# Kernel tuning notes

Measured on AMD Instinct MI355X. Metric: run time of the kernel, lower is better.

Reference implementation:

```python
import jax, jax.numpy as jnp
import numpy as np

B, C, H, W, L, R = 1, 32, 96, 128, 2, 3
N = 2 * R + 1
EPS = 1e-5


def conv2d(x, w, stride=1, pad=1):
    return jax.lax.conv_general_dilated(
        x, w, (stride, stride), ((pad, pad), (pad, pad)),
        dimension_numbers=('NCHW', 'OIHW', 'NCHW'))


def conv_transpose2d(x, w, stride=2, pad=1):
    # torch ConvTranspose2d semantics; w: [Cin, Cout, kH, kW]
    kh, kw = w.shape[2], w.shape[3]
    wf = jnp.flip(w, (2, 3)).transpose(1, 0, 2, 3)  # [Cout, Cin, kh, kw]
    return jax.lax.conv_general_dilated(
        x, wf, (1, 1),
        ((kh - 1 - pad, kh - 1 - pad), (kw - 1 - pad, kw - 1 - pad)),
        lhs_dilation=(stride, stride),
        dimension_numbers=('NCHW', 'OIHW', 'NCHW'))


def bnorm(x, s, b, m, v):
    # inference-mode BatchNorm2d (fixed running stats)
    inv = s * jax.lax.rsqrt(v + EPS)
    return x * inv[None, :, None, None] + (b - m * inv)[None, :, None, None]


def grid_sample(img, grid):
    # bilinear, align_corners=True, padding_mode='zeros'
    # img [B,C,H,W], grid [B,Hg,Wg,2] (x,y) in [-1,1]
    Bi, Ci, Hi, Wi = img.shape
    gx = (grid[..., 0] + 1.0) * 0.5 * (Wi - 1)
    gy = (grid[..., 1] + 1.0) * 0.5 * (Hi - 1)
    x0 = jnp.floor(gx)
    y0 = jnp.floor(gy)
    wx = (gx - x0)[:, None]  # [B,1,Hg,Wg]
    wy = (gy - y0)[:, None]

    def tap(yf, xf):
        valid = (xf >= 0) & (xf <= Wi - 1) & (yf >= 0) & (yf <= Hi - 1)
        xc = jnp.clip(xf, 0, Wi - 1).astype(jnp.int32)
        yc = jnp.clip(yf, 0, Hi - 1).astype(jnp.int32)
        v = jax.vmap(lambda im, y, x: im[:, y, x])(img, yc, xc)  # [B,C,Hg,Wg]
        return v * valid[:, None].astype(img.dtype)

    v00 = tap(y0, x0)
    v01 = tap(y0, x0 + 1)
    v10 = tap(y0 + 1, x0)
    v11 = tap(y0 + 1, x0 + 1)
    return (v00 * (1 - wx) * (1 - wy) + v01 * wx * (1 - wy)
            + v10 * (1 - wx) * wy + v11 * wx * wy)


def _forward(fmap1_0, fmap1_1, fmap2_0, fmap2_1, coords,
             cw1, cw2, cw3, cw4, ctw5, cw6, cb6,
             bn1s, bn1b, bn1m, bn1v, bn2s, bn2b, bn2m, bn2v,
             bn3s, bn3b, bn3m, bn3v, bn4s, bn4b, bn4m, bn4v,
             bn5s, bn5b, bn5m, bn5v, dap_w):
    n = N
    dx = jnp.linspace(-R, R, n)
    delta = jnp.stack(jnp.meshgrid(dx, dx, indexing='ij'), axis=-1)  # [n,n,2]
    b, _, h, w = coords.shape
    cp = coords.transpose(0, 2, 3, 1)  # [b,h,w,2] (x,y)
    bns = ((bn1s, bn1b, bn1m, bn1v), (bn2s, bn2b, bn2m, bn2v),
           (bn3s, bn3b, bn3m, bn3v), (bn4s, bn4b, bn4m, bn4v),
           (bn5s, bn5b, bn5m, bn5v))
    out = []
    for i, (f1, f2) in enumerate(((fmap1_0, fmap2_0), (fmap1_1, fmap2_1))):
        c, h2, w2 = f1.shape[1], f1.shape[2], f1.shape[3]
        # [b,n,h,n,w,2]: first n axis pairs with h, second with w (as in torch view)
        cent = cp[:, None, :, None, :, :] / (2.0 ** i) + delta[None, :, None, :, None, :]
        gx = 2.0 * cent[..., 0] / (w2 - 1) - 1.0
        gy = 2.0 * cent[..., 1] / (h2 - 1) - 1.0
        grid = jnp.stack([gx, gy], -1).reshape(b, n * h, n * w, 2)
        f2s = grid_sample(f2, grid).reshape(b, c, n, h, n, w)
        f2s = f2s.transpose(0, 2, 4, 1, 3, 5)  # [b,du,dv,c,h,w]
        f1e = jnp.broadcast_to(f1[:, None, None], (b, n, n, c, h, w))
        x = jnp.concatenate([f1e, f2s], axis=3).reshape(b * n * n, 2 * c, h, w)
        # MatchingNet (DICL): conv-bn-relu stack, stride-2 down + transposed up
        x = jax.nn.relu(bnorm(conv2d(x, cw1[i]), *(p[i] for p in bns[0])))
        x = jax.nn.relu(bnorm(conv2d(x, cw2[i], stride=2), *(p[i] for p in bns[1])))
        x = jax.nn.relu(bnorm(conv2d(x, cw3[i]), *(p[i] for p in bns[2])))
        x = jax.nn.relu(bnorm(conv2d(x, cw4[i]), *(p[i] for p in bns[3])))
        x = jax.nn.relu(bnorm(conv_transpose2d(x, ctw5[i]), *(p[i] for p in bns[4])))
        x = conv2d(x, cw6[i]) + cb6[i][None, :, None, None]  # [b*n*n,1,h,w]
        cost = x.reshape(b, n * n, h, w)
        # DisplacementAwareProjection: 1x1 conv over the 49 displacement channels
        cost = jnp.einsum('pq,bqhw->bphw', dap_w[i], cost)
        out.append(cost)
    return jnp.concatenate(out, axis=1)  # [b, L*(2r+1)^2, h, w]


def setup_inputs():
    key = jax.random.key(0)
    ks = jax.random.split(key, 40)

    def rn(k, shape, scale=1.0):
        return jax.random.normal(k, shape, jnp.float32) * scale

    inp = {}
    inp['fmap1_0'] = rn(ks[0], (B, C, H, W))
    inp['fmap2_0'] = rn(ks[1], (B, C, H, W))
    inp['fmap1_1'] = rn(ks[2], (B, C, H, W))
    inp['fmap2_1'] = rn(ks[3], (B, C, H, W))
    gy, gx = jnp.meshgrid(jnp.arange(H, dtype=jnp.float32),
                          jnp.arange(W, dtype=jnp.float32), indexing='ij')
    base = jnp.stack([gx, gy], 0)[None]  # [1,2,H,W] (x,y) pixel coords
    inp['coords'] = base + rn(ks[4], (B, 2, H, W), 2.0)

    def cw(k, co, ci, kk):
        return rn(k, (L, co, ci, kk, kk), 1.0 / np.sqrt(ci * kk * kk))

    inp['cw1'] = cw(ks[5], 96, 2 * C, 3)
    inp['cw2'] = cw(ks[6], 128, 96, 3)
    inp['cw3'] = cw(ks[7], 128, 128, 3)
    inp['cw4'] = cw(ks[8], 64, 128, 3)
    inp['ctw5'] = rn(ks[9], (L, 64, 32, 4, 4), 1.0 / np.sqrt(64 * 16))
    inp['cw6'] = cw(ks[10], 1, 32, 3)
    inp['cb6'] = rn(ks[11], (L, 1), 0.1)
    for j, ch in enumerate((96, 128, 128, 64, 32), start=1):
        k4 = jax.random.split(ks[11 + j], 4)
        inp['bn%ds' % j] = 1.0 + rn(k4[0], (L, ch), 0.1)
        inp['bn%db' % j] = rn(k4[1], (L, ch), 0.1)
        inp['bn%dm' % j] = rn(k4[2], (L, ch), 0.1)
        inp['bn%dv' % j] = 1.0 + rn(k4[3], (L, ch), 0.1) ** 2
    # DAP identity init
    inp['dap_w'] = jnp.tile(jnp.eye(N * N, dtype=jnp.float32)[None], (L, 1, 1))
    return inp


def reference(fmap1_0, fmap1_1, fmap2_0, fmap2_1, coords,
              cw1, cw2, cw3, cw4, ctw5, cw6, cb6,
              bn1s, bn1b, bn1m, bn1v, bn2s, bn2b, bn2m, bn2v,
              bn3s, bn3b, bn3m, bn3v, bn4s, bn4b, bn4m, bn4v,
              bn5s, bn5b, bn5m, bn5v, dap_w):
    return _forward(fmap1_0, fmap1_1, fmap2_0, fmap2_1, coords,
                    cw1, cw2, cw3, cw4, ctw5, cw6, cb6,
                    bn1s, bn1b, bn1m, bn1v, bn2s, bn2b, bn2m, bn2v,
                    bn3s, bn3b, bn3m, bn3v, bn4s, bn4b, bn4m, bn4v,
                    bn5s, bn5b, bn5m, bn5v, dap_w)
```

## Files before the change

kernel.cpp:

```cpp
#include <hip/hip_runtime.h>

#define EPSF 1e-5f

typedef __attribute__((ext_vector_type(8))) short short8;
typedef __attribute__((ext_vector_type(4))) float f32x4;

__device__ __forceinline__ ushort f2bf(float x) {
    union { float f; unsigned u; } c; c.f = x;
    unsigned r = c.u + 0x7FFF + ((c.u >> 16) & 1);
    return (ushort)(r >> 16);
}
__device__ __forceinline__ float bf2f(ushort b) {
    union { unsigned u; float f; } c; c.u = ((unsigned)b) << 16;
    return c.f;
}
__device__ __forceinline__ int swz(int a) {
    return a ^ (((a >> 7) & 7) << 4);
}


__global__ __launch_bounds__(256) void k_repack_conv(
    const float* __restrict__ src, ushort* __restrict__ dst, int CO, int CI)
{
    int idx = blockIdx.x * 256 + threadIdx.x;
    if (idx >= CO * CI * 9) return;
    int co = idx / (CI * 9);
    int rem = idx % (CI * 9);
    int ci = rem / 9, tap = rem % 9;
    dst[((size_t)tap * CO + co) * CI + ci] = f2bf(src[idx]);
}

__global__ __launch_bounds__(256) void k_repack_ct(
    const float* __restrict__ src, ushort* __restrict__ dst)
{
    int idx = blockIdx.x * 256 + threadIdx.x;
    if (idx >= 4 * 4 * 32 * 64) return;
    int ci = idx & 63;
    int t = idx >> 6;
    int co = t & 31; t >>= 5;
    int tap = t & 3;
    int parity = t >> 2;
    int ph = parity >> 1, pw = parity & 1;
    int a = tap >> 1, b = tap & 1;
    int kh = ((ph + 1) & 1) + 2 * a;
    int kw = ((pw + 1) & 1) + 2 * b;
    dst[idx] = f2bf(src[((ci * 32 + co) * 4 + kh) * 4 + kw]);
}

__global__ __launch_bounds__(256) void k_pack_f1(
    const float* __restrict__ f1_0, const float* __restrict__ f1_1,
    ushort* __restrict__ xf1)
{
    const int sp = blockIdx.x * 256 + threadIdx.x;
    const int l = blockIdx.z;
    const float* f1 = l ? f1_1 : f1_0;
    ushort* dst = xf1 + (size_t)l * 393216 + (size_t)sp * 32;
    #pragma unroll
    for (int g = 0; g < 4; ++g) {
        uint4 pk;
        uint* pw_ = (uint*)&pk;
        #pragma unroll
        for (int q = 0; q < 4; ++q) {
            int c = g * 8 + q * 2;
            pw_[q] = (uint)f2bf(f1[(size_t)c * 12288 + sp])
                   | ((uint)f2bf(f1[(size_t)(c + 1) * 12288 + sp]) << 16);
        }
        *(uint4*)(dst + g * 8) = pk;
    }
}

__global__ __launch_bounds__(256) void k_sample_nhwc(
    const float* __restrict__ f2_0, const float* __restrict__ f2_1,
    const float* __restrict__ coords, ushort* __restrict__ x0s, int d0)
{
    const int HW = 12288;
    const int sp = blockIdx.x * 256 + threadIdx.x;
    const int slot = blockIdx.z;
    const int p = d0 + slot;
    const int l = p / 49;
    const int d = p - l * 49;
    const int du = d / 7, dv = d % 7;
    const float inv_scale = l ? 0.5f : 1.0f;
    const float* f2 = l ? f2_1 : f2_0;

    float cx = coords[sp] * inv_scale + (float)(du - 3);
    float cy = coords[HW + sp] * inv_scale + (float)(dv - 3);
    float xf = floorf(cx), yf = floorf(cy);
    float wx = cx - xf, wy = cy - yf;
    int xi = (int)xf, yi = (int)yf;
    float vx0 = (xf >= 0.f && xf <= 127.f) ? 1.f : 0.f;
    float vx1 = (xf + 1.f >= 0.f && xf + 1.f <= 127.f) ? 1.f : 0.f;
    float vy0 = (yf >= 0.f && yf <= 95.f) ? 1.f : 0.f;
    float vy1 = (yf + 1.f >= 0.f && yf + 1.f <= 95.f) ? 1.f : 0.f;
    int x0i = min(max(xi, 0), 127), x1i = min(max(xi + 1, 0), 127);
    int y0i = min(max(yi, 0), 95),  y1i = min(max(yi + 1, 0), 95);
    float w00 = (1.f - wx) * (1.f - wy) * vx0 * vy0;
    float w01 = wx * (1.f - wy) * vx1 * vy0;
    float w10 = (1.f - wx) * wy * vx0 * vy1;
    float w11 = wx * wy * vx1 * vy1;
    int o00 = y0i * 128 + x0i, o01 = y0i * 128 + x1i;
    int o10 = y1i * 128 + x0i, o11 = y1i * 128 + x1i;

    ushort* dst = x0s + ((size_t)slot * HW + sp) * 32;
    #pragma unroll
    for (int g = 0; g < 4; ++g) {
        uint4 pk;
        uint* pw_ = (uint*)&pk;
        #pragma unroll
        for (int q = 0; q < 4; ++q) {
            uint wv = 0;
            #pragma unroll
            for (int h = 0; h < 2; ++h) {
                int c = g * 8 + q * 2 + h;
                const float* fc = f2 + (size_t)c * HW;
                float s = w00 * fc[o00] + w01 * fc[o01] + w10 * fc[o10] + w11 * fc[o11];
                wv |= ((uint)f2bf(s)) << (16 * h);
            }
            pw_[q] = wv;
        }
        *(uint4*)(dst + g * 8) = pk;
    }
}

template <int EPI>
__global__ __launch_bounds__(512, 2) void k_conv1(
    const ushort* __restrict__ in,
    ushort* __restrict__ out,
    const ushort* __restrict__ wbase,
    const float* __restrict__ p1,
    const float* __restrict__ bs0, const float* __restrict__ bb0,
    const float* __restrict__ bm0, const float* __restrict__ bv0,
    int d0, int koff)
{
    constexpr int AB = 10 * 66 * 64;
    constexpr int PB = 3 * 48 * 64;
    constexpr int SA = 6;
    __shared__ __align__(16) char smem[AB + 2 * PB];
    char* As = smem;

    const int tid = threadIdx.x;
    const int lane = tid & 63, wid = tid >> 6;
    const int lr = lane & 15, kg = lane >> 4;
    const int bx = blockIdx.x;
    const int rt = bx >> 1, ct = bx & 1;
    const int r0 = rt * 8, c0 = ct * 64;
    const int y = blockIdx.y;
    const int co0 = y * 48;
    const int slot = blockIdx.z;
    const int l = EPI ? slot : (d0 + slot) / 49;

    const ushort* ib = in + (size_t)slot * 12288 * 32;
    const ushort* wl = wbase + (size_t)l * (9 * 96 * 64);
    const short8 z8 = {0, 0, 0, 0, 0, 0, 0, 0};

    #pragma unroll
    for (int i = 0; i < SA; ++i) {
        int lin = i * 8192 + tid * 16;
        if (lin < AB) {
            int pos = lin >> 6;
            int prow = (pos * 994) >> 16;
            int pcol = pos - prow * 66;
            int grow = r0 - 1 + prow, gcol = c0 - 1 + pcol;
            bool ok = ((unsigned)grow < 96u) && ((unsigned)gcol < 128u);
            short8 v = z8;
            if (ok) v = *(const short8*)(ib + (grow * 128 + gcol) * 32 + ((lin & 63) >> 1));
            *(short8*)(As + swz(lin)) = v;
        }
    }

    int boff[2]; unsigned bmask = 0;
    #pragma unroll
    for (int i = 0; i < 2; ++i) {
        int lin = i * 8192 + tid * 16;
        if (lin < PB) bmask |= 1u << i;
        int lc = min(lin, PB - 16);
        int rowidx = lc >> 6;
        int tpg = rowidx / 48;
        int r = rowidx - tpg * 48;
        boff[i] = (tpg * 96 + co0 + r) * 64 + koff + ((lc & 63) >> 1);
    }
    short8 stgB[2];
    auto loadB = [&](int pg) {
        const ushort* src = wl + pg * (3 * 96 * 64);
        #pragma unroll
        for (int i = 0; i < 2; ++i)
            if ((bmask >> i) & 1) stgB[i] = *(const short8*)(src + boff[i]);
    };
    auto writeB = [&](int pg) {
        char* Bs = smem + AB + (pg & 1) * PB;
        #pragma unroll
        for (int i = 0; i < 2; ++i) {
            int lin = i * 8192 + tid * 16;
            if ((bmask >> i) & 1) *(short8*)(Bs + swz(lin)) = stgB[i];
        }
    };

    f32x4 acc[4][3];
    if constexpr (EPI == 0) {
        const float* pl = p1 + (size_t)l * 1179648
                        + ((size_t)((bx * 2 + y) * 512 + tid)) * 48;
        #pragma unroll
        for (int mf = 0; mf < 4; ++mf)
            #pragma unroll
            for (int nf = 0; nf < 3; ++nf)
                acc[mf][nf] = *(const f32x4*)(pl + (mf * 3 + nf) * 4);
    } else {
        #pragma unroll
        for (int mf = 0; mf < 4; ++mf)
            #pragma unroll
            for (int nf = 0; nf < 3; ++nf)
                acc[mf][nf] = (f32x4){0.f, 0.f, 0.f, 0.f};
    }

    loadB(0);
    writeB(0);
    __syncthreads();

    #pragma unroll
    for (int ps = 0; ps < 3; ++ps) {
        if (ps < 2) loadB(ps + 1);
        const char* Bs = smem + AB + (ps & 1) * PB;
        #pragma unroll
        for (int kw = 0; kw < 3; ++kw) {
            short8 a[4];
            #pragma unroll
            for (int mf = 0; mf < 4; ++mf) {
                int sp = (wid + ps) * 66 + mf * 16 + lr + kw;
                a[mf] = *(const short8*)(As + swz(sp * 64 + kg * 16));
            }
            #pragma unroll
            for (int nf = 0; nf < 3; ++nf) {
                short8 b = *(const short8*)(Bs + swz((kw * 48 + nf * 16 + lr) * 64 + kg * 16));
                #pragma unroll
                for (int mf = 0; mf < 4; ++mf)
                    acc[mf][nf] = __builtin_amdgcn_mfma_f32_16x16x32_bf16(
                        a[mf], b, acc[mf][nf], 0, 0, 0);
            }
        }
        __syncthreads();
        if (ps < 2) { writeB(ps + 1); __syncthreads(); }
    }

    if constexpr (EPI == 1) {
        float* of = (float*)out + (size_t)l * 1179648
                  + ((size_t)((bx * 2 + y) * 512 + tid)) * 48;
        #pragma unroll
        for (int mf = 0; mf < 4; ++mf)
            #pragma unroll
            for (int nf = 0; nf < 3; ++nf)
                *(f32x4*)(of + (mf * 3 + nf) * 4) = acc[mf][nf];
    } else {
        const float* bs = bs0 + l * 96;
        const float* bb = bb0 + l * 96;
        const float* bm = bm0 + l * 96;
        const float* bv = bv0 + l * 96;
        ushort* ob = out + (size_t)slot * 12288 * 96;
        const int orow = r0 + wid;
        #pragma unroll
        for (int nf = 0; nf < 3; ++nf) {
            const int col = co0 + nf * 16 + lr;
            const float inv = bs[col] * rsqrtf(bv[col] + EPSF);
            const float beta = bb[col] - bm[col] * inv;
            #pragma unroll
            for (int mf = 0; mf < 4; ++mf) {
                #pragma unroll
                for (int j = 0; j < 4; ++j) {
                    int ocol = c0 + mf * 16 + kg * 4 + j;
                    float yv = fmaxf(fmaf(acc[mf][nf][j], inv, beta), 0.f);
                    ob[((size_t)orow * 128 + ocol) * 96 + col] = f2bf(yv);
                }
            }
        }
    }
}

template <int CIN, int COUT, int IH, int IW>
__global__ __launch_bounds__(512, 4) void k_conv_lds8s(
    const ushort* __restrict__ in, ushort* __restrict__ out,
    const ushort* __restrict__ wbase, int wlstride,
    const float* __restrict__ bs0, const float* __restrict__ bb0,
    const float* __restrict__ bm0, const float* __restrict__ bv0, int d0)
{
    constexpr int CCs = CIN / 32;
    constexpr int AB = 10 * 66 * 64;
    constexpr int PB = 3 * 64 * 64;
    constexpr int SA = 6, SB = 2;
    constexpr int NPH = 3 * CCs;
    __shared__ __align__(16) char smem[AB + 2 * PB];
    char* As = smem;

    const int tid = threadIdx.x;
    const int lane = tid & 63, wid = tid >> 6;
    const int lr = lane & 15, kg = lane >> 4;
    const int r0 = (int)blockIdx.x * 8;
    const int co0 = (int)blockIdx.y * 64;
    const int slot = blockIdx.z;
    const int l = (d0 + slot) / 49;

    int aoff[SA]; unsigned awr = 0, avalid = 0;
    #pragma unroll
    for (int i = 0; i < SA; ++i) {
        int lin = i * 8192 + tid * 16;
        bool wr = lin < AB;
        int linc = wr ? lin : 0;
        int pos = linc >> 6;
        int prow = (pos * 994) >> 16;
        int pcol = pos - prow * 66;
        int grow = r0 - 1 + prow, gcol = pcol - 1;
        bool ok = wr && ((unsigned)grow < (unsigned)IH) && ((unsigned)gcol < (unsigned)IW);
        if (wr) awr |= 1u << i;
        if (ok) avalid |= 1u << i;
        int growc = min(max(grow, 0), IH - 1), gcolc = min(max(gcol, 0), IW - 1);
        aoff[i] = (growc * IW + gcolc) * CIN + ((linc & 63) >> 1);
    }
    int boff[SB]; unsigned bmask = 0;
    #pragma unroll
    for (int i = 0; i < SB; ++i) {
        int lin = i * 8192 + tid * 16;
        if (lin < PB) bmask |= 1u << i;
        int lc = min(lin, PB - 16);
        int rowidx = lc >> 6;
        int tpg = rowidx >> 6, r = rowidx & 63;
        boff[i] = (tpg * COUT + co0 + r) * CIN + ((lc & 63) >> 1);
    }

    const ushort* ib = in + (size_t)slot * IH * IW * CIN;
    const ushort* wl = wbase + (size_t)l * wlstride;
    const short8 z8 = {0, 0, 0, 0, 0, 0, 0, 0};

    auto stageA = [&](int cc) {
        #pragma unroll
        for (int i = 0; i < SA; ++i) {
            int lin = i * 8192 + tid * 16;
            if ((awr >> i) & 1) {
                short8 v = z8;
                if ((avalid >> i) & 1)
                    v = *(const short8*)(ib + aoff[i] + cc * 32);
                *(short8*)(As + swz(lin)) = v;
            }
        }
    };
    short8 stgB[SB];
    auto loadB = [&](int ps) {
        int pg = ps % 3, cc = ps / 3;
        const ushort* src = wl + pg * (3 * COUT * CIN) + cc * 32;
        #pragma unroll
        for (int i = 0; i < SB; ++i)
            if ((bmask >> i) & 1) stgB[i] = *(const short8*)(src + boff[i]);
    };
    auto writeB = [&](int ps) {
        char* Bs = smem + AB + (ps & 1) * PB;
        #pragma unroll
        for (int i = 0; i < SB; ++i) {
            int lin = i * 8192 + tid * 16;
            if ((bmask >> i) & 1) *(short8*)(Bs + swz(lin)) = stgB[i];
        }
    };

    f32x4 acc[4][4];
    #pragma unroll
    for (int mf = 0; mf < 4; ++mf)
        #pragma unroll
        for (int nf = 0; nf < 4; ++nf)
            acc[mf][nf] = (f32x4){0.f, 0.f, 0.f, 0.f};

    stageA(0);
    loadB(0); writeB(0);
    __syncthreads();

    #pragma unroll 1
    for (int ps = 0; ps < NPH; ++ps) {
        const int pg = ps % 3;
        const bool hasNext = (ps + 1 < NPH);
        if (hasNext) loadB(ps + 1);

        const char* Bs = smem + AB + (ps & 1) * PB;
        #pragma unroll
        for (int kw = 0; kw < 3; ++kw) {
            short8 a[4];
            #pragma unroll
            for (int mf = 0; mf < 4; ++mf) {
                int sp = (wid + pg) * 66 + mf * 16 + lr + kw;
                a[mf] = *(const short8*)(As + swz(sp * 64 + kg * 16));
            }
            #pragma unroll
            for (int nf = 0; nf < 4; ++nf) {
                short8 b = *(const short8*)(Bs + swz((kw * 64 + nf * 16 + lr) * 64 + kg * 16));
                #pragma unroll
                for (int mf = 0; mf < 4; ++mf)
                    acc[mf][nf] = __builtin_amdgcn_mfma_f32_16x16x32_bf16(
                        a[mf], b, acc[mf][nf], 0, 0, 0);
            }
        }

        __syncthreads();
        if (hasNext) {
            writeB(ps + 1);
            if (pg == 2) stageA(ps / 3 + 1);
            __syncthreads();
        }
    }

    const float* bs = bs0 + l * COUT;
    const float* bb = bb0 + l * COUT;
    const float* bm = bm0 + l * COUT;
    const float* bv = bv0 + l * COUT;
    ushort* ob = out + (size_t)slot * IH * IW * COUT;
    const int orow = r0 + wid;
    #pragma unroll
    for (int nf = 0; nf < 4; ++nf) {
        const int col = co0 + nf * 16 + lr;
        const float inv = bs[col] * rsqrtf(bv[col] + EPSF);
        const float beta = bb[col] - bm[col] * inv;
        #pragma unroll
        for (int mf = 0; mf < 4; ++mf) {
            #pragma unroll
            for (int j = 0; j < 4; ++j) {
                int ocol = mf * 16 + kg * 4 + j;
                float y = fmaxf(fmaf(acc[mf][nf][j], inv, beta), 0.f);
                ob[((size_t)orow * IW + ocol) * COUT + col] = f2bf(y);
            }
        }
    }
}

__global__ __launch_bounds__(512, 4) void k_conv_s2_8(
    const ushort* __restrict__ in, ushort* __restrict__ out,
    const ushort* __restrict__ wbase, int wlstride,
    const float* __restrict__ bs0, const float* __restrict__ bb0,
    const float* __restrict__ bm0, const float* __restrict__ bv0, int d0)
{
    constexpr int AB = 9 * 66 * 64;
    constexpr int PB = 3 * 128 * 64;
    constexpr int SA = 5;
    constexpr int SB = 3;
    constexpr int NPH = 9;
    __shared__ __align__(16) char smem[AB + PB];
    char* As = smem;

    const int tid = threadIdx.x;
    const int lane = tid & 63, wid = tid >> 6;
    const int lr = lane & 15, kg = lane >> 4;
    const int mw = wid >> 2;
    const int cw = wid & 3;
    const int bx = blockIdx.x;
    const int rt = bx >> 1, ct = bx & 1;
    const int r0 = rt * 4, oc0 = ct * 32;
    const int slot = blockIdx.z;
    const int l = (d0 + slot) / 49;

    int aoff[SA]; unsigned awr = 0, avalid = 0;
    #pragma unroll
    for (int i = 0; i < SA; ++i) {
        int lin = i * 8192 + tid * 16;
        bool wr = lin < AB;
        int linc = wr ? lin : 0;
        int pos = linc >> 6;
        int prow = (pos * 994) >> 16;
        int pcol = pos - prow * 66;
        int grow = 2 * r0 - 1 + prow, gcol = 2 * oc0 - 1 + pcol;
        bool ok = wr && ((unsigned)grow < 96u) && ((unsigned)gcol < 128u);
        if (wr) awr |= 1u << i;
        if (ok) avalid |= 1u << i;
        int growc = min(max(grow, 0), 95), gcolc = min(max(gcol, 0), 127);
        aoff[i] = (growc * 128 + gcolc) * 96 + ((linc & 63) >> 1);
    }
    int boff[SB];
    #pragma unroll
    for (int i = 0; i < SB; ++i) {
        int lin = i * 8192 + tid * 16;
        int rowidx = lin >> 6;
        int tpg = rowidx >> 7, r = rowidx & 127;
        boff[i] = (tpg * 128 + r) * 96 + ((lin & 63) >> 1);
    }

    const ushort* ib = in + (size_t)slot * 12288 * 96;
    const ushort* wl = wbase + (size_t)l * wlstride;
    const short8 z8 = {0, 0, 0, 0, 0, 0, 0, 0};

    auto stageA = [&](int cc) {
        #pragma unroll
        for (int i = 0; i < SA; ++i) {
            int lin = i * 8192 + tid * 16;
            if ((awr >> i) & 1) {
                short8 v = z8;
                if ((avalid >> i) & 1)
                    v = *(const short8*)(ib + aoff[i] + cc * 32);
                *(short8*)(As + swz(lin)) = v;
            }
        }
    };
    short8 stgB[SB];
    auto loadB = [&](int ps) {
        int pg = ps % 3, cc = ps / 3;
        const ushort* src = wl + pg * (3 * 128 * 96) + cc * 32;
        #pragma unroll
        for (int i = 0; i < SB; ++i)
            stgB[i] = *(const short8*)(src + boff[i]);
    };
    auto writeB = [&]() {
        char* Bs = smem + AB;
        #pragma unroll
        for (int i = 0; i < SB; ++i) {
            int lin = i * 8192 + tid * 16;
            *(short8*)(Bs + swz(lin)) = stgB[i];
        }
    };

    f32x4 acc[4][2];
    #pragma unroll
    for (int mf = 0; mf < 4; ++mf)
        #pragma unroll
        for (int nf = 0; nf < 2; ++nf)
            acc[mf][nf] = (f32x4){0.f, 0.f, 0.f, 0.f};

    stageA(0);
    loadB(0); writeB();
    __syncthreads();

    #pragma unroll 1
    for (int ps = 0; ps < NPH; ++ps) {
        const int pg = ps % 3;
        const bool hasNext = (ps + 1 < NPH);
        if (hasNext) loadB(ps + 1);

        const char* Bs = smem + AB;
        #pragma unroll
        for (int kw = 0; kw < 3; ++kw) {
            short8 a[4];
            #pragma unroll
            for (int mf = 0; mf < 4; ++mf) {
                int pos = (2 * (mw * 2 + (mf >> 1)) + pg) * 66
                        + 2 * ((mf & 1) * 16 + lr) + kw;
                a[mf] = *(const short8*)(As + swz(pos * 64 + kg * 16));
            }
            #pragma unroll
            for (int nf = 0; nf < 2; ++nf) {
                int rb = kw * 128 + cw * 32 + nf * 16 + lr;
                short8 b = *(const short8*)(Bs + swz(rb * 64 + kg * 16));
                #pragma unroll
                for (int mf = 0; mf < 4; ++mf)
                    acc[mf][nf] = __builtin_amdgcn_mfma_f32_16x16x32_bf16(
                        a[mf], b, acc[mf][nf], 0, 0, 0);
            }
        }

        __syncthreads();
        if (hasNext) {
            writeB();
            if (pg == 2) stageA(ps / 3 + 1);
            __syncthreads();
        }
    }

    const float* bs = bs0 + l * 128;
    const float* bb = bb0 + l * 128;
    const float* bm = bm0 + l * 128;
    const float* bv = bv0 + l * 128;
    ushort* ob = out + (size_t)slot * 3072 * 128;
    #pragma unroll
    for (int nf = 0; nf < 2; ++nf) {
        const int col = cw * 32 + nf * 16 + lr;
        const float inv = bs[col] * rsqrtf(bv[col] + EPSF);
        const float beta = bb[col] - bm[col] * inv;
        #pragma unroll
        for (int mf = 0; mf < 4; ++mf) {
            const int orow = r0 + mw * 2 + (mf >> 1);
            #pragma unroll
            for (int j = 0; j < 4; ++j) {
                int ocol = oc0 + (mf & 1) * 16 + kg * 4 + j;
                float y = fmaxf(fmaf(acc[mf][nf][j], inv, beta), 0.f);
                ob[((size_t)orow * 64 + ocol) * 128 + col] = f2bf(y);
            }
        }
    }
}

__global__ __launch_bounds__(512, 4) void k_convt_lds(
    const ushort* __restrict__ in, ushort* __restrict__ out,
    const ushort* __restrict__ wbase,
    const float* __restrict__ bs0, const float* __restrict__ bb0,
    const float* __restrict__ bm0, const float* __restrict__ bv0, int d0)
{
    constexpr int AB = 10 * 66 * 64;
    constexpr int PB = 4 * 32 * 64;
    constexpr int SA = 6;
    __shared__ __align__(16) char smem[AB + 2 * PB];
    char* As = smem;

    const int tid = threadIdx.x;
    const int lane = tid & 63, wid = tid >> 6;
    const int lr = lane & 15, kg = lane >> 4;
    const int q0 = (int)blockIdx.x * 8;
    const int parity = blockIdx.y;
    const int ph = parity >> 1, pw = parity & 1;
    const int slot = blockIdx.z;
    const int l = (d0 + slot) / 49;

    int aoff[SA]; unsigned awr = 0, avalid = 0;
    #pragma unroll
    for (int i = 0; i < SA; ++i) {
        int lin = i * 8192 + tid * 16;
        bool wr = lin < AB;
        int linc = wr ? lin : 0;
        int pos = linc >> 6;
        int prow = (pos * 994) >> 16;
        int pcol = pos - prow * 66;
        int grow = q0 - 1 + prow, gcol = pcol - 1;
        bool ok = wr && ((unsigned)grow < 48u) && ((unsigned)gcol < 64u);
        if (wr) awr |= 1u << i;
        if (ok) avalid |= 1u << i;
        int growc = min(max(grow, 0), 47), gcolc = min(max(gcol, 0), 63);
        aoff[i] = (growc * 64 + gcolc) * 64 + ((linc & 63) >> 1);
    }
    int boffB;
    {
        int lin = tid * 16;
        int rowidx = lin >> 6;
        int tap = rowidx >> 5, co = rowidx & 31;
        boffB = ((parity * 4 + tap) * 32 + co) * 64 + ((lin & 63) >> 1);
    }

    const ushort* ib = in + (size_t)slot * 3072 * 64;
    const ushort* wl = wbase + (size_t)l * (16 * 32 * 64);
    const short8 z8 = {0, 0, 0, 0, 0, 0, 0, 0};

    auto stageA = [&](int cc) {
        #pragma unroll
        for (int i = 0; i < SA; ++i) {
            int lin = i * 8192 + tid * 16;
            if ((awr >> i) & 1) {
                short8 v = z8;
                if ((avalid >> i) & 1)
                    v = *(const short8*)(ib + aoff[i] + cc * 32);
                *(short8*)(As + swz(lin)) = v;
            }
        }
    };
    short8 stgB;
    auto loadB = [&](int cc) {
        stgB = *(const short8*)(wl + boffB + cc * 32);
    };
    auto writeB = [&](int cc) {
        char* Bs = smem + AB + (cc & 1) * PB;
        *(short8*)(Bs + swz(tid * 16)) = stgB;
    };

    f32x4 acc[4][2];
    #pragma unroll
    for (int mf = 0; mf < 4; ++mf)
        #pragma unroll
        for (int nf = 0; nf < 2; ++nf)
            acc[mf][nf] = (f32x4){0.f, 0.f, 0.f, 0.f};

    stageA(0);
    loadB(0); writeB(0);
    __syncthreads();

    #pragma unroll 1
    for (int cc = 0; cc < 2; ++cc) {
        if (cc == 0) loadB(1);
        const char* Bs = smem + AB + (cc & 1) * PB;
        #pragma unroll
        for (int a = 0; a < 2; ++a) {
            #pragma unroll
            for (int b2 = 0; b2 < 2; ++b2) {
                const int tap = a * 2 + b2;
                short8 av[4];
                #pragma unroll
                for (int mf = 0; mf < 4; ++mf) {
                    int pos = (wid + 1 + ph - a) * 66 + mf * 16 + lr + pw - b2 + 1;
                    av[mf] = *(const short8*)(As + swz(pos * 64 + kg * 16));
                }
                #pragma unroll
                for (int nf = 0; nf < 2; ++nf) {
                    short8 b = *(const short8*)(Bs
                        + swz((tap * 32 + nf * 16 + lr) * 64 + kg * 16));
                    #pragma unroll
                    for (int mf = 0; mf < 4; ++mf)
                        acc[mf][nf] = __builtin_amdgcn_mfma_f32_16x16x32_bf16(
                            av[mf], b, acc[mf][nf], 0, 0, 0);
                }
            }
        }
        __syncthreads();
        if (cc == 0) {
            writeB(1);
            stageA(1);
            __syncthreads();
        }
    }

    const float* bs = bs0 + l * 32;
    const float* bb = bb0 + l * 32;
    const float* bm = bm0 + l * 32;
    const float* bv = bv0 + l * 32;
    ushort* ob = out + (size_t)slot * 12288 * 32;
    const size_t rowb = (size_t)(2 * (q0 + wid) + ph) * 128;
    #pragma unroll
    for (int nf = 0; nf < 2; ++nf) {
        const int col = nf * 16 + lr;
        const float inv = bs[col] * rsqrtf(bv[col] + EPSF);
        const float beta = bb[col] - bm[col] * inv;
        #pragma unroll
        for (int mf = 0; mf < 4; ++mf) {
            #pragma unroll
            for (int j = 0; j < 4; ++j) {
                int r = mf * 16 + kg * 4 + j;
                float y = fmaxf(fmaf(acc[mf][nf][j], inv, beta), 0.f);
                ob[(rowb + 2 * r + pw) * 32 + col] = f2bf(y);
            }
        }
    }
}

__global__ __launch_bounds__(256) void k_conv6(
    const ushort* __restrict__ x5, float* __restrict__ cost,
    const float* __restrict__ w0, const float* __restrict__ cb6, int d0)
{
    const int sp = blockIdx.x * 256 + threadIdx.x;
    const int slot = blockIdx.z;
    const int p = d0 + slot;
    const int l = p / 49;
    const float* w = w0 + l * 288;
    const int oh = sp >> 7, ow = sp & 127;
    float acc = 0.f;
    #pragma unroll
    for (int kh = 0; kh < 3; ++kh) {
        const int ih = oh - 1 + kh;
        if (ih < 0 || ih >= 96) continue;
        #pragma unroll
        for (int kw = 0; kw < 3; ++kw) {
            const int iw = ow - 1 + kw;
            if (iw < 0 || iw >= 128) continue;
            const ushort* q = x5 + ((size_t)slot * 12288 + ih * 128 + iw) * 32;
            const int tap = kh * 3 + kw;
            #pragma unroll
            for (int g = 0; g < 4; ++g) {
                uint4 v = *(const uint4*)(q + g * 8);
                const uint* vw = (const uint*)&v;
                #pragma unroll
                for (int t = 0; t < 4; ++t) {
                    int ci = g * 8 + t * 2;
                    acc = fmaf(bf2f((ushort)(vw[t] & 0xFFFF)), w[ci * 9 + tap], acc);
                    acc = fmaf(bf2f((ushort)(vw[t] >> 16)), w[(ci + 1) * 9 + tap], acc);
                }
            }
        }
    }
    cost[(size_t)p * 12288 + sp] = acc + cb6[l];
}

__global__ __launch_bounds__(256) void k_dap(
    const float* __restrict__ cost, const float* __restrict__ dw,
    float* __restrict__ out)
{
    const int sp = blockIdx.x * 256 + threadIdx.x;
    const int p = blockIdx.y;
    const float* dr = dw + p * 49;
    float acc = 0.f;
    #pragma unroll
    for (int q = 0; q < 49; ++q)
        acc = fmaf(dr[q], cost[(size_t)q * 12288 + sp], acc);
    out[(size_t)p * 12288 + sp] = acc;
}

extern "C" void kernel_launch(void* const* d_in, const int* in_sizes, int n_in,
                              void* d_out, int out_size, void* d_ws, size_t ws_size,
                              hipStream_t stream)
{
    const float* fm1_0 = (const float*)d_in[0];
    const float* fm2_0 = (const float*)d_in[1];
    const float* fm1_1 = (const float*)d_in[2];
    const float* fm2_1 = (const float*)d_in[3];
    const float* coords = (const float*)d_in[4];
    const float* cw1  = (const float*)d_in[5];
    const float* cw2  = (const float*)d_in[6];
    const float* cw3  = (const float*)d_in[7];
    const float* cw4  = (const float*)d_in[8];
    const float* ctw5 = (const float*)d_in[9];
    const float* cw6  = (const float*)d_in[10];
    const float* cb6  = (const float*)d_in[11];
    const float* bn[5][4];
    for (int j = 0; j < 5; ++j)
        for (int k = 0; k < 4; ++k)
            bn[j][k] = (const float*)d_in[12 + j * 4 + k];
    const float* dap = (const float*)d_in[32];
    float* out = (float*)d_out;

    const size_t A_US = 393216;
    const size_t B_US = 1179648;
    const size_t XF1 = 2 * 393216;
    const size_t W1 = 9 * 96 * 64, W2 = 9 * 128 * 96, W3 = 9 * 128 * 128;
    const size_t W4 = 9 * 64 * 128, W5 = 16 * 32 * 64;
    const size_t W_US = 2 * (W1 + W2 + W3 + W4 + W5);
    const size_t P1F = 2 * (size_t)24 * 2 * 512 * 48;
    const size_t COSTF = (size_t)98 * 12288;

    int DC = 1;
    for (int cand : {98, 66, 49, 42, 33, 25, 17, 13, 9, 7, 5, 3, 2, 1}) {
        size_t need = (A_US + B_US) * (size_t)cand * 2 + (XF1 + W_US) * 2
                    + (P1F + COSTF) * 4 + 4096;
        if (need <= ws_size) { DC = cand; break; }
    }

    ushort* bufA = (ushort*)d_ws;
    ushort* bufB = bufA + A_US * DC;
    ushort* xf1 = bufB + B_US * DC;
    ushort* wp = xf1 + XF1;
    ushort* wr1 = wp; wp += 2 * W1;
    ushort* wr2 = wp; wp += 2 * W2;
    ushort* wr3 = wp; wp += 2 * W3;
    ushort* wr4 = wp; wp += 2 * W4;
    ushort* wr5 = wp; wp += 2 * W5;
    float* P1 = (float*)wp;
    float* cost = P1 + P1F;

    for (int l = 0; l < 2; ++l) {
        k_repack_conv<<<dim3(216), 256, 0, stream>>>(cw1 + (size_t)l * W1, wr1 + l * W1, 96, 64);
        k_repack_conv<<<dim3(432), 256, 0, stream>>>(cw2 + (size_t)l * W2, wr2 + l * W2, 128, 96);
        k_repack_conv<<<dim3(576), 256, 0, stream>>>(cw3 + (size_t)l * W3, wr3 + l * W3, 128, 128);
        k_repack_conv<<<dim3(288), 256, 0, stream>>>(cw4 + (size_t)l * W4, wr4 + l * W4, 64, 128);
        k_repack_ct<<<dim3(128), 256, 0, stream>>>(ctw5 + (size_t)l * W5, wr5 + l * W5);
    }

    k_pack_f1<<<dim3(48, 1, 2), 256, 0, stream>>>(fm1_0, fm1_1, xf1);
    k_conv1<1><<<dim3(24, 2, 2), 512, 0, stream>>>(
        xf1, (ushort*)P1, wr1, nullptr,
        bn[0][0], bn[0][1], bn[0][2], bn[0][3], 0, 0);

    for (int d0 = 0; d0 < 98; d0 += DC) {
        const int ndd = min(DC, 98 - d0);
        k_sample_nhwc<<<dim3(48, 1, ndd), 256, 0, stream>>>(
            fm2_0, fm2_1, coords, bufA, d0);
        k_conv1<0><<<dim3(24, 2, ndd), 512, 0, stream>>>(
            bufA, bufB, wr1, P1,
            bn[0][0], bn[0][1], bn[0][2], bn[0][3], d0, 32);
        k_conv_s2_8<<<dim3(24, 1, ndd), 512, 0, stream>>>(bufB, bufA, wr2, (int)W2,
                bn[1][0], bn[1][1], bn[1][2], bn[1][3], d0);
        k_conv_lds8s<128, 128, 48, 64>
            <<<dim3(6, 2, ndd), 512, 0, stream>>>(bufA, bufB, wr3, (int)W3,
                bn[2][0], bn[2][1], bn[2][2], bn[2][3], d0);
        k_conv_lds8s<128, 64, 48, 64>
            <<<dim3(6, 1, ndd), 512, 0, stream>>>(bufB, bufA, wr4, (int)W4,
                bn[3][0], bn[3][1], bn[3][2], bn[3][3], d0);
        k_convt_lds<<<dim3(6, 4, ndd), 512, 0, stream>>>(bufA, bufB, wr5,
                bn[4][0], bn[4][1], bn[4][2], bn[4][3], d0);
        k_conv6<<<dim3(48, 1, ndd), 256, 0, stream>>>(
            bufB, cost, cw6, cb6, d0);
    }
    for (int l = 0; l < 2; ++l)
        k_dap<<<dim3(48, 49), 256, 0, stream>>>(
            cost + (size_t)l * 49 * 12288, dap + (size_t)l * 49 * 49,
            out + (size_t)l * 49 * 12288);
}
```

Before: 734.4 us.

## Retile conv1 to cover all output channels per block; prefetch A in strided conv

conv1 blocks now cover 4 output rows and all 96 output channels, with the 8 waves split into row and channel halves, instead of 8 rows by 48 channels. The input halo tile is staged once per block rather than once per channel half, at the cost of a larger weight tile and a grid twice as long. In the stride-2 conv, the next input chunk is now loaded into registers before compute and written to LDS afterward, so the global load latency can overlap the MFMA work. Its occupancy hint drops from 4 to 2 blocks per CU to make room for the extra registers.

After: 725.4 us. No clear change (-1.2%).

```diff
diff --git a/kernel.cpp b/kernel.cpp
--- a/kernel.cpp
+++ b/kernel.cpp
@@ -132,9 +132,10 @@
     const float* __restrict__ bm0, const float* __restrict__ bv0,
     int d0, int koff)
 {
-    constexpr int AB = 10 * 66 * 64;
-    constexpr int PB = 3 * 48 * 64;
-    constexpr int SA = 6;
+    constexpr int AB = 6 * 66 * 64;
+    constexpr int PB = 3 * 96 * 64;
+    constexpr int SA = 4;
+    constexpr int SB = 3;
     __shared__ __align__(16) char smem[AB + 2 * PB];
     char* As = smem;
 
@@ -143,9 +144,8 @@
     const int lr = lane & 15, kg = lane >> 4;
     const int bx = blockIdx.x;
     const int rt = bx >> 1, ct = bx & 1;
-    const int r0 = rt * 8, c0 = ct * 64;
-    const int y = blockIdx.y;
-    const int co0 = y * 48;
+    const int r0 = rt * 4, c0 = ct * 64;
+    const int wr = wid >> 1, coh = wid & 1;
     const int slot = blockIdx.z;
     const int l = EPI ? slot : (d0 + slot) / 49;
 
@@ -168,28 +168,28 @@
         }
     }
 
-    int boff[2]; unsigned bmask = 0;
-    #pragma unroll
-    for (int i = 0; i < 2; ++i) {
+    int boff[SB]; unsigned bmask = 0;
+    #pragma unroll
+    for (int i = 0; i < SB; ++i) {
         int lin = i * 8192 + tid * 16;
         if (lin < PB) bmask |= 1u << i;
         int lc = min(lin, PB - 16);
         int rowidx = lc >> 6;
-        int tpg = rowidx / 48;
-        int r = rowidx - tpg * 48;
-        boff[i] = (tpg * 96 + co0 + r) * 64 + koff + ((lc & 63) >> 1);
-    }
-    short8 stgB[2];
+        int tpg = rowidx / 96;
+        int r = rowidx - tpg * 96;
+        boff[i] = (tpg * 96 + r) * 64 + koff + ((lc & 63) >> 1);
+    }
+    short8 stgB[SB];
     auto loadB = [&](int pg) {
         const ushort* src = wl + pg * (3 * 96 * 64);
         #pragma unroll
-        for (int i = 0; i < 2; ++i)
+        for (int i = 0; i < SB; ++i)
             if ((bmask >> i) & 1) stgB[i] = *(const short8*)(src + boff[i]);
     };
     auto writeB = [&](int pg) {
         char* Bs = smem + AB + (pg & 1) * PB;
         #pragma unroll
-        for (int i = 0; i < 2; ++i) {
+        for (int i = 0; i < SB; ++i) {
             int lin = i * 8192 + tid * 16;
             if ((bmask >> i) & 1) *(short8*)(Bs + swz(lin)) = stgB[i];
         }
@@ -198,7 +198,7 @@
     f32x4 acc[4][3];
     if constexpr (EPI == 0) {
         const float* pl = p1 + (size_t)l * 1179648
-                        + ((size_t)((bx * 2 + y) * 512 + tid)) * 48;
+                        + ((size_t)(bx * 512 + tid)) * 48;
         #pragma unroll
         for (int mf = 0; mf < 4; ++mf)
             #pragma unroll
@@ -225,12 +225,13 @@
             short8 a[4];
             #pragma unroll
             for (int mf = 0; mf < 4; ++mf) {
-                int sp = (wid + ps) * 66 + mf * 16 + lr + kw;
+                int sp = (wr + ps) * 66 + mf * 16 + lr + kw;
                 a[mf] = *(const short8*)(As + swz(sp * 64 + kg * 16));
             }
             #pragma unroll
             for (int nf = 0; nf < 3; ++nf) {
-                short8 b = *(const short8*)(Bs + swz((kw * 48 + nf * 16 + lr) * 64 + kg * 16));
+                int rb = kw * 96 + coh * 48 + nf * 16 + lr;
+                short8 b = *(const short8*)(Bs + swz(rb * 64 + kg * 16));
                 #pragma unroll
                 for (int mf = 0; mf < 4; ++mf)
                     acc[mf][nf] = __builtin_amdgcn_mfma_f32_16x16x32_bf16(
@@ -243,7 +244,7 @@
 
     if constexpr (EPI == 1) {
         float* of = (float*)out + (size_t)l * 1179648
-                  + ((size_t)((bx * 2 + y) * 512 + tid)) * 48;
+                  + ((size_t)(bx * 512 + tid)) * 48;
         #pragma unroll
         for (int mf = 0; mf < 4; ++mf)
             #pragma unroll
@@ -255,10 +256,10 @@
         const float* bm = bm0 + l * 96;
         const float* bv = bv0 + l * 96;
         ushort* ob = out + (size_t)slot * 12288 * 96;
-        const int orow = r0 + wid;
+        const int orow = r0 + wr;
         #pragma unroll
         for (int nf = 0; nf < 3; ++nf) {
-            const int col = co0 + nf * 16 + lr;
+            const int col = coh * 48 + nf * 16 + lr;
             const float inv = bs[col] * rsqrtf(bv[col] + EPSF);
             const float beta = bb[col] - bm[col] * inv;
             #pragma unroll
@@ -424,7 +425,7 @@
     }
 }
 
-__global__ __launch_bounds__(512, 4) void k_conv_s2_8(
+__global__ __launch_bounds__(512, 2) void k_conv_s2_8(
     const ushort* __restrict__ in, ushort* __restrict__ out,
     const ushort* __restrict__ wbase, int wlstride,
     const float* __restrict__ bs0, const float* __restrict__ bb0,
@@ -478,19 +479,22 @@
     const ushort* wl = wbase + (size_t)l * wlstride;
     const short8 z8 = {0, 0, 0, 0, 0, 0, 0, 0};
 
-    auto stageA = [&](int cc) {
+    short8 stgA[SA], stgB[SB];
+    auto loadA = [&](int cc) {
+        #pragma unroll
+        for (int i = 0; i < SA; ++i) {
+            if ((avalid >> i) & 1) stgA[i] = *(const short8*)(ib + aoff[i] + cc * 32);
+            else stgA[i] = z8;
+        }
+    };
+    auto writeA = [&]() {
         #pragma unroll
         for (int i = 0; i < SA; ++i) {
             int lin = i * 8192 + tid * 16;
-            if ((awr >> i) & 1) {
-                short8 v = z8;
-                if ((avalid >> i) & 1)
-                    v = *(const short8*)(ib + aoff[i] + cc * 32);
-                *(short8*)(As + swz(lin)) = v;
-            }
-        }
-    };
-    short8 stgB[SB];
+            if ((awr >> i) & 1)
+                *(short8*)(As + swz(lin)) = stgA[i];
+        }
+    };
     auto loadB = [&](int ps) {
         int pg = ps % 3, cc = ps / 3;
         const ushort* src = wl + pg * (3 * 128 * 96) + cc * 32;
@@ -514,15 +518,17 @@
         for (int nf = 0; nf < 2; ++nf)
             acc[mf][nf] = (f32x4){0.f, 0.f, 0.f, 0.f};
 
-    stageA(0);
-    loadB(0); writeB();
+    loadA(0); loadB(0);
+    writeA(); writeB();
     __syncthreads();
 
     #pragma unroll 1
     for (int ps = 0; ps < NPH; ++ps) {
         const int pg = ps % 3;
         const bool hasNext = (ps + 1 < NPH);
+        const bool newA = (pg == 2) && hasNext;
         if (hasNext) loadB(ps + 1);
+        if (newA) loadA(ps / 3 + 1);
 
         const char* Bs = smem + AB;
         #pragma unroll
@@ -548,7 +554,7 @@
         __syncthreads();
         if (hasNext) {
             writeB();
-            if (pg == 2) stageA(ps / 3 + 1);
+            if (newA) writeA();
             __syncthreads();
         }
     }
@@ -794,7 +800,7 @@
     const size_t W1 = 9 * 96 * 64, W2 = 9 * 128 * 96, W3 = 9 * 128 * 128;
     const size_t W4 = 9 * 64 * 128, W5 = 16 * 32 * 64;
     const size_t W_US = 2 * (W1 + W2 + W3 + W4 + W5);
-    const size_t P1F = 2 * (size_t)24 * 2 * 512 * 48;
+    const size_t P1F = 2 * (size_t)48 * 512 * 48;
     const size_t COSTF = (size_t)98 * 12288;
 
     int DC = 1;
@@ -825,7 +831,7 @@
     }
 
     k_pack_f1<<<dim3(48, 1, 2), 256, 0, stream>>>(fm1_0, fm1_1, xf1);
-    k_conv1<1><<<dim3(24, 2, 2), 512, 0, stream>>>(
+    k_conv1<1><<<dim3(48, 1, 2), 512, 0, stream>>>(
         xf1, (ushort*)P1, wr1, nullptr,
         bn[0][0], bn[0][1], bn[0][2], bn[0][3], 0, 0);
 
@@ -833,7 +839,7 @@
         const int ndd = min(DC, 98 - d0);
         k_sample_nhwc<<<dim3(48, 1, ndd), 256, 0, stream>>>(
             fm2_0, fm2_1, coords, bufA, d0);
-        k_conv1<0><<<dim3(24, 2, ndd), 512, 0, stream>>>(
+        k_conv1<0><<<dim3(48, 1, ndd), 512, 0, stream>>>(
             bufA, bufB, wr1, P1,
             bn[0][0], bn[0][1], bn[0][2], bn[0][3], d0, 32);
         k_conv_s2_8<<<dim3(24, 1, ndd), 512, 0, stream>>>(bufB, bufA, wr2, (int)W2,
```
